# Kernel tuning notes

Hardware: AMD Instinct MI355X
Metric: run time of the kernel (lower is better)

The kernel has to match this reference:

```python
import jax, jax.numpy as jnp
import numpy as np

N = 4096  # num_dev == num_task (required by elementwise msg computation)
D = 64    # embed_dim


def setup_inputs() -> dict:
    key = jax.random.key(0)
    ks = jax.random.split(key, 10)
    return {
        "embed": jax.random.normal(ks[0], (2 * N, D), jnp.float32),
        "adj_collab": jnp.zeros((N, N), jnp.float32),   # only .shape[0] is used
        "adj_interact": jnp.zeros((N, N), jnp.float32),  # unused in forward body
        "adj_similar": jnp.zeros((N, N), jnp.float32),   # unused in forward body
        "collab_score": jax.random.normal(ks[1], (N, N), jnp.float32),
        "interact_score": jax.random.normal(ks[2], (N, N), jnp.float32),
        "similar_score": jax.random.normal(ks[3], (N, N), jnp.float32),
        "deg_dev": jax.random.uniform(ks[4], (N,), jnp.float32, 1.0, 100.0),
        "deg_task": jax.random.uniform(ks[5], (N,), jnp.float32, 1.0, 100.0),
        "W1": jax.random.normal(ks[6], (D, D), jnp.float32) / np.sqrt(D).astype(np.float32),
        "b1": jnp.zeros((D,), jnp.float32),
        "W2": jax.random.normal(ks[7], (D, D), jnp.float32) / np.sqrt(D).astype(np.float32),
        "b2": jnp.zeros((D,), jnp.float32),
        "W3": jax.random.normal(ks[8], (D, D), jnp.float32) / np.sqrt(D).astype(np.float32),
        "b3": jnp.zeros((D,), jnp.float32),
    }


def _linear(x, W, b):
    # torch nn.Linear: x @ W.T + b
    return x @ W.T + b


def _calc_attention(src, dst, rel_score, src_deg, dst_deg):
    # msg = dst + src*dst ; per-row dot <src, msg> ; degree + sqrt(d) scaling ; softmax
    msg = dst + src * dst                      # [N, D]
    dot = jnp.sum(src * msg, axis=-1)          # [N]
    scale = dot / (jnp.sqrt(src_deg * dst_deg + 1e-8) * jnp.sqrt(jnp.float32(src.shape[-1])))
    att = jax.nn.softmax(rel_score * scale, axis=-1)  # [N, N] (scale broadcasts over columns)
    return att, msg


def reference(embed, adj_collab, adj_interact, adj_similar,
              collab_score, interact_score, similar_score,
              deg_dev, deg_task, W1, b1, W2, b2, W3, b3):
    num_dev = adj_collab.shape[0]
    dev = embed[:num_dev]       # [N, D]
    task = embed[num_dev:]      # [N, D]

    collab_att, collab_msg = _calc_attention(dev, dev, collab_score, deg_dev, deg_dev)
    collab_prop = collab_att @ _linear(collab_msg, W1, b1)

    interact_att, interact_msg = _calc_attention(dev, task, interact_score, deg_dev, deg_task)
    interact_prop = interact_att @ _linear(interact_msg, W2, b2)

    dev_prop = jax.nn.leaky_relu(_linear(dev + collab_prop + interact_prop, W3, b3), 0.2)

    similar_att, _similar_msg = _calc_attention(task, task, similar_score, deg_task, deg_task)
    similar_prop = similar_att @ _linear(task, W3, b3)  # note: original uses W3(task_embed), not the msg
    task_prop = jax.nn.leaky_relu(_linear(task + similar_prop, W3, b3), 0.2)

    # dropout omitted (eval mode / identity)
    return jnp.concatenate([dev_prop, task_prop], axis=0)
```

## Files before the change

### kernel.cpp

```cpp
#include <hip/hip_runtime.h>
#include <math.h>

#define N 4096
#define D 64
#define NSLICE 4
#define JLEN 1024
#define CH 32
#define NCHUNK 32
#define SH 44.0f

#define S_OFF   0
#define MT_OFF  24576
#define E_OFF   36864
#define SCL_OFF 40960
#define LDS_BYTES 45056

typedef short bf16x8 __attribute__((ext_vector_type(8)));
typedef float f32x4  __attribute__((ext_vector_type(4)));

__device__ __forceinline__ unsigned short f2bf(float x) {
    unsigned int u = __float_as_uint(x);
    u += 0x7FFFu + ((u >> 16) & 1u);
    return (unsigned short)(u >> 16);
}
__device__ __forceinline__ float bf2f(unsigned short h) {
    return __uint_as_float(((unsigned int)h) << 16);
}

__device__ __forceinline__ void gld16(const void* g, void* l) {
    __builtin_amdgcn_global_load_lds(
        (const __attribute__((address_space(1))) void*)g,
        (__attribute__((address_space(3))) void*)l,
        16, 0, 0);
}

__device__ __forceinline__ void lds_barrier() {
    asm volatile("s_waitcnt lgkmcnt(0)" ::: "memory");
    __builtin_amdgcn_s_barrier();
    asm volatile("" ::: "memory");
}
__device__ __forceinline__ void plain_barrier() {
    asm volatile("" ::: "memory");
    __builtin_amdgcn_s_barrier();
    asm volatile("" ::: "memory");
}

__global__ __launch_bounds__(256) void prep_kernel(
    const float* __restrict__ embed,
    const float* __restrict__ degd, const float* __restrict__ degt,
    const float* __restrict__ W1, const float* __restrict__ b1,
    const float* __restrict__ W2, const float* __restrict__ b2,
    const float* __restrict__ W3, const float* __restrict__ b3,
    float* __restrict__ scale, unsigned short* __restrict__ Mt)
{
    const int rel = blockIdx.y;
    const float* W  = (rel == 0) ? W1 : (rel == 1 ? W2 : W3);
    const float* bb = (rel == 0) ? b1 : (rel == 1 ? b2 : b3);
    __shared__ float Wl[D][D + 1];
    __shared__ float xr[4][D];
    const int tid = threadIdx.x;
    for (int idx = tid; idx < D * D; idx += 256)
        Wl[idx >> 6][idx & 63] = W[idx];
    const int w = tid >> 6, d = tid & 63;
    const int i = blockIdx.x * 4 + w;

    float msg, term, xsrc, dga, dgb;
    if (rel == 0) {
        float s = embed[(size_t)i * D + d];
        msg = s + s * s; term = s * msg; xsrc = msg;
        dga = degd[i]; dgb = degd[i];
    } else if (rel == 1) {
        float s = embed[(size_t)i * D + d];
        float t = embed[(size_t)(N + i) * D + d];
        msg = t + s * t; term = s * msg; xsrc = msg;
        dga = degd[i]; dgb = degt[i];
    } else {
        float t = embed[(size_t)(N + i) * D + d];
        msg = t + t * t; term = t * msg; xsrc = t;
        dga = degt[i]; dgb = degt[i];
    }
    float dot = term;
    #pragma unroll
    for (int mm = 1; mm < 64; mm <<= 1) dot += __shfl_xor(dot, mm);
    if (d == 0)
        scale[rel * N + i] = dot / (sqrtf(dga * dgb + 1e-8f) * 8.0f);

    xr[w][d] = xsrc;
    __syncthreads();
    float o = bb[d];
    #pragma unroll 8
    for (int k = 0; k < D; ++k) o += xr[w][k] * Wl[d][k];
    Mt[((size_t)rel * D + d) * N + i] = f2bf(o);
}

__global__ __launch_bounds__(256, 3) void attn_kernel(
    const float* __restrict__ S0, const float* __restrict__ S1, const float* __restrict__ S2,
    const float* __restrict__ scale, const unsigned short* __restrict__ Mt,
    unsigned short* __restrict__ Up, float* __restrict__ lp)
{
    __shared__ __align__(16) char LDS[LDS_BYTES];
    const int rg = blockIdx.x, rel = blockIdx.y, sl = blockIdx.z;
    const float* S = (rel == 0) ? S0 : (rel == 1 ? S1 : S2);
    const unsigned short* Mtr = Mt + (size_t)rel * D * N;
    const int tid = threadIdx.x;
    const int lane = tid & 63, wave = tid >> 6;
    const int row = tid >> 2, q = tid & 3;
    const int j0 = sl * JLEN;

    const int srow = tid >> 3, sslot = tid & 7;
    const int sx = (sslot ^ (srow & 7)) * 4;
    const float* s0p = S + (size_t)(rg * 64 + srow) * N + j0 + sx;
    const float* s1p = S + (size_t)(rg * 64 + 32 + srow) * N + j0 + sx;
    const unsigned short* mtp = Mtr + (size_t)(tid & 63) * N + j0 + (tid >> 6) * 8;
    char* sldsw = LDS + S_OFF + wave * 1024;
    char* mldsw = LDS + MT_OFF + wave * 1024;

#define ISSUE(cc, bb) do {                                      \
        gld16(s0p + (cc) * CH, sldsw + (bb) * 8192);            \
        gld16(s1p + (cc) * CH, sldsw + (bb) * 8192 + 4096);     \
        gld16(mtp + (cc) * CH, mldsw + (bb) * 4096);            \
    } while (0)

    for (int k = tid; k < JLEN; k += 256)
        *(float*)(LDS + SCL_OFF + k * 4) = scale[rel * N + j0 + k];
    asm volatile("" ::: "memory");
    ISSUE(0, 0);
    ISSUE(1, 1);
    lds_barrier();

    const int wbase = wave * 16;
    const int lrow  = lane & 15;
    const int lk    = lane >> 4;
    float l = 0.f;
    f32x4 acc[4];
    #pragma unroll
    for (int ct = 0; ct < 4; ++ct) {
        acc[ct][0] = 0.f; acc[ct][1] = 0.f; acc[ct][2] = 0.f; acc[ct][3] = 0.f;
    }

    int bc = 0;
    for (int c = 0; c < NCHUNK; ++c) {
        if (c < NCHUNK - 1) asm volatile("s_waitcnt vmcnt(3)" ::: "memory");
        else                asm volatile("s_waitcnt vmcnt(0)" ::: "memory");
        plain_barrier();

        if (c + 2 < NCHUNK) {
            int bn = bc + 2; if (bn >= 3) bn -= 3;
            ISSUE(c + 2, bn);
        }

        {
            const char* sb = LDS + S_OFF + bc * 8192;
            const int r7 = row & 7;
            const f32x4 va = *(const f32x4*)(sb + row * 128 + (((2 * q)     ^ r7) << 4));
            const f32x4 vb = *(const f32x4*)(sb + row * 128 + (((2 * q + 1) ^ r7) << 4));
            const f32x4 ca = *(const f32x4*)(LDS + SCL_OFF + c * 128 + q * 32);
            const f32x4 cb = *(const f32x4*)(LDS + SCL_OFF + c * 128 + q * 32 + 16);
            float e[8];
            e[0] = __expf(fmaf(va[0], ca[0], -SH));
            e[1] = __expf(fmaf(va[1], ca[1], -SH));
            e[2] = __expf(fmaf(va[2], ca[2], -SH));
            e[3] = __expf(fmaf(va[3], ca[3], -SH));
            e[4] = __expf(fmaf(vb[0], cb[0], -SH));
            e[5] = __expf(fmaf(vb[1], cb[1], -SH));
            e[6] = __expf(fmaf(vb[2], cb[2], -SH));
            e[7] = __expf(fmaf(vb[3], cb[3], -SH));
            #pragma unroll
            for (int k = 0; k < 8; ++k) l += e[k];
            union { unsigned short h[8]; uint4 v; } pk;
            #pragma unroll
            for (int k = 0; k < 8; ++k) pk.h[k] = f2bf(e[k]);
            *(uint4*)(LDS + E_OFF + ((q * 64 + row) << 4)) = pk.v;
        }

        lds_barrier();

        {
            const char* mb = LDS + MT_OFF + bc * 4096;
            const bf16x8 a = *(const bf16x8*)(LDS + E_OFF + ((lk * 64 + wbase + lrow) << 4));
            #pragma unroll
            for (int ct = 0; ct < 4; ++ct) {
                const bf16x8 b = *(const bf16x8*)(mb + ((lk * 64 + ct * 16 + lrow) << 4));
                acc[ct] = __builtin_amdgcn_mfma_f32_16x16x32_bf16(a, b, acc[ct], 0, 0, 0);
            }
        }

        bc = bc + 1; if (bc == 3) bc = 0;
    }
#undef ISSUE

    unsigned short* R = (unsigned short*)LDS;
    #pragma unroll
    for (int ct = 0; ct < 4; ++ct)
        #pragma unroll
        for (int r = 0; r < 4; ++r) {
            const int ri = wbase + lk * 4 + r;
            R[ri * 64 + ct * 16 + lrow] = f2bf(acc[ct][r]);
        }
    lds_barrier();
    const size_t pbase = (size_t)((rel * 64 + rg) * NSLICE + sl);
    unsigned short* up = Up + pbase * 4096;
    {
        const uint4* src = (const uint4*)R;
        uint4*       dst = (uint4*)up;
        dst[tid]       = src[tid];
        dst[256 + tid] = src[256 + tid];
    }
    l += __shfl_xor(l, 1);
    l += __shfl_xor(l, 2);
    if (q == 0) lp[pbase * 64 + row] = l;
}

__device__ __forceinline__ float combine_row(
    const unsigned short* __restrict__ Up, const float* __restrict__ lp,
    int rel, int i, int d)
{
    const int rg = i >> 6, r = i & 63;
    const int base = (rel * 64 + rg) * NSLICE;
    float lt = 0.f, u = 0.f;
    #pragma unroll
    for (int p = 0; p < NSLICE; ++p) {
        lt += lp[(base + p) * 64 + r];
        u  += bf2f(Up[(size_t)(base + p) * 4096 + r * 64 + d]);
    }
    return u / lt;
}

__global__ __launch_bounds__(256) void final_kernel(
    const float* __restrict__ embed,
    const unsigned short* __restrict__ Up, const float* __restrict__ lp,
    const float* __restrict__ W3, const float* __restrict__ b3,
    float* __restrict__ out)
{
    __shared__ float Wl[D][D + 1];
    __shared__ float xs[4][D];
    const int tid = threadIdx.x;
    for (int idx = tid; idx < D * D; idx += 256)
        Wl[idx >> 6][idx & 63] = W3[idx];
    const int w = tid >> 6, d = tid & 63;
    const int g = blockIdx.x * 4 + w;

    float x = embed[(size_t)g * D + d];
    if (g < N) {
        x += combine_row(Up, lp, 0, g, d);
        x += combine_row(Up, lp, 1, g, d);
    } else {
        x += combine_row(Up, lp, 2, g - N, d);
    }
    xs[w][d] = x;
    __syncthreads();
    float o = b3[d];
    #pragma unroll 8
    for (int k = 0; k < D; ++k) o += xs[w][k] * Wl[d][k];
    o = (o > 0.f) ? o : 0.2f * o;
    out[(size_t)g * D + d] = o;
}

extern "C" void kernel_launch(void* const* d_in, const int* in_sizes, int n_in,
                              void* d_out, int out_size, void* d_ws, size_t ws_size,
                              hipStream_t stream)
{
    const float* embed = (const float*)d_in[0];
    const float* Sc   = (const float*)d_in[4];
    const float* Si   = (const float*)d_in[5];
    const float* Ss   = (const float*)d_in[6];
    const float* degd = (const float*)d_in[7];
    const float* degt = (const float*)d_in[8];
    const float* W1 = (const float*)d_in[9];
    const float* b1 = (const float*)d_in[10];
    const float* W2 = (const float*)d_in[11];
    const float* b2 = (const float*)d_in[12];
    const float* W3 = (const float*)d_in[13];
    const float* b3 = (const float*)d_in[14];
    float* out = (float*)d_out;

    float* ws    = (float*)d_ws;
    float* scale = ws;
    float* lp    = ws + 12288;
    unsigned short* Mt = (unsigned short*)(lp + 49152);
    unsigned short* Up = Mt + 786432;

    prep_kernel<<<dim3(N / 4, 3), 256, 0, stream>>>(
        embed, degd, degt, W1, b1, W2, b2, W3, b3, scale, Mt);
    attn_kernel<<<dim3(64, 3, NSLICE), 256, 0, stream>>>(
        Sc, Si, Ss, scale, Mt, Up, lp);
    final_kernel<<<dim3(2 * N / 4), 256, 0, stream>>>(
        embed, Up, lp, W3, b3, out);
}
```

Baseline: 59.97 us.

## Double column slices, deepen score prefetch to 4 buffers, swizzle E tile

Splits the column range into 8 slices instead of 4, so the attention grid has twice as many blocks, each covering half the columns. The score tiles get a 4-deep ring buffer with a 3-chunk lookahead, while the message tiles keep a 3-deep ring, and the wait counts are adjusted to match. The bf16 exponent tile in LDS is XOR-swizzled to reduce bank conflicts. The extra slices double the partial outputs that the final kernel must reduce, and the larger LDS footprint may lower occupancy.

Result: slower. 62.86 us (+4.8%).

```diff
diff --git a/kernel.cpp b/kernel.cpp
--- a/kernel.cpp
+++ b/kernel.cpp
@@ -3,17 +3,17 @@
 
 #define N 4096
 #define D 64
-#define NSLICE 4
-#define JLEN 1024
+#define NSLICE 8
+#define JLEN 512
 #define CH 32
-#define NCHUNK 32
+#define NCHUNK 16
 #define SH 44.0f
 
 #define S_OFF   0
-#define MT_OFF  24576
-#define E_OFF   36864
-#define SCL_OFF 40960
-#define LDS_BYTES 45056
+#define MT_OFF  32768
+#define E_OFF   45056
+#define SCL_OFF 49152
+#define LDS_BYTES 51200
 
 typedef short bf16x8 __attribute__((ext_vector_type(8)));
 typedef float f32x4  __attribute__((ext_vector_type(4)));
@@ -111,21 +111,22 @@
     const int sx = (sslot ^ (srow & 7)) * 4;
     const float* s0p = S + (size_t)(rg * 64 + srow) * N + j0 + sx;
     const float* s1p = S + (size_t)(rg * 64 + 32 + srow) * N + j0 + sx;
-    const unsigned short* mtp = Mtr + (size_t)(tid & 63) * N + j0 + (tid >> 6) * 8;
+    const unsigned short* mtp = Mtr + (size_t)(tid & 63) * N + j0 + wave * 8;
     char* sldsw = LDS + S_OFF + wave * 1024;
     char* mldsw = LDS + MT_OFF + wave * 1024;
 
-#define ISSUE(cc, bb) do {                                      \
-        gld16(s0p + (cc) * CH, sldsw + (bb) * 8192);            \
-        gld16(s1p + (cc) * CH, sldsw + (bb) * 8192 + 4096);     \
-        gld16(mtp + (cc) * CH, mldsw + (bb) * 4096);            \
+#define ISSUE_S(cc, bb) do {                                \
+        gld16(s0p + (cc) * CH, sldsw + (bb) * 8192);        \
+        gld16(s1p + (cc) * CH, sldsw + (bb) * 8192 + 4096); \
     } while (0)
+#define ISSUE_M(cc, bb) gld16(mtp + (cc) * CH, mldsw + (bb) * 4096)
 
     for (int k = tid; k < JLEN; k += 256)
         *(float*)(LDS + SCL_OFF + k * 4) = scale[rel * N + j0 + k];
     asm volatile("" ::: "memory");
-    ISSUE(0, 0);
-    ISSUE(1, 1);
+    ISSUE_M(0, 0); ISSUE_S(0, 0);
+    ISSUE_M(1, 1); ISSUE_S(1, 1);
+    ISSUE_S(2, 2);
     lds_barrier();
 
     const int wbase = wave * 16;
@@ -138,19 +139,18 @@
         acc[ct][0] = 0.f; acc[ct][1] = 0.f; acc[ct][2] = 0.f; acc[ct][3] = 0.f;
     }
 
-    int bc = 0;
+    int bm = 0;
     for (int c = 0; c < NCHUNK; ++c) {
-        if (c < NCHUNK - 1) asm volatile("s_waitcnt vmcnt(3)" ::: "memory");
-        else                asm volatile("s_waitcnt vmcnt(0)" ::: "memory");
+        if (c < NCHUNK - 2)       asm volatile("s_waitcnt vmcnt(5)" ::: "memory");
+        else if (c == NCHUNK - 2) asm volatile("s_waitcnt vmcnt(3)" ::: "memory");
+        else                      asm volatile("s_waitcnt vmcnt(0)" ::: "memory");
         plain_barrier();
 
-        if (c + 2 < NCHUNK) {
-            int bn = bc + 2; if (bn >= 3) bn -= 3;
-            ISSUE(c + 2, bn);
-        }
+        if (c + 2 < NCHUNK) { int t = bm + 2; if (t >= 3) t -= 3; ISSUE_M(c + 2, t); }
+        if (c + 3 < NCHUNK) ISSUE_S(c + 3, (c + 3) & 3);
 
         {
-            const char* sb = LDS + S_OFF + bc * 8192;
+            const char* sb = LDS + S_OFF + (c & 3) * 8192;
             const int r7 = row & 7;
             const f32x4 va = *(const f32x4*)(sb + row * 128 + (((2 * q)     ^ r7) << 4));
             const f32x4 vb = *(const f32x4*)(sb + row * 128 + (((2 * q + 1) ^ r7) << 4));
@@ -170,14 +170,15 @@
             union { unsigned short h[8]; uint4 v; } pk;
             #pragma unroll
             for (int k = 0; k < 8; ++k) pk.h[k] = f2bf(e[k]);
-            *(uint4*)(LDS + E_OFF + ((q * 64 + row) << 4)) = pk.v;
+            *(uint4*)(LDS + E_OFF + ((q * 64 + (row ^ (2 * q))) << 4)) = pk.v;
         }
 
         lds_barrier();
 
         {
-            const char* mb = LDS + MT_OFF + bc * 4096;
-            const bf16x8 a = *(const bf16x8*)(LDS + E_OFF + ((lk * 64 + wbase + lrow) << 4));
+            const char* mb = LDS + MT_OFF + bm * 4096;
+            const bf16x8 a = *(const bf16x8*)(
+                LDS + E_OFF + ((lk * 64 + ((wbase + lrow) ^ (2 * lk))) << 4));
             #pragma unroll
             for (int ct = 0; ct < 4; ++ct) {
                 const bf16x8 b = *(const bf16x8*)(mb + ((lk * 64 + ct * 16 + lrow) << 4));
@@ -185,9 +186,10 @@
             }
         }
 
-        bc = bc + 1; if (bc == 3) bc = 0;
-    }
-#undef ISSUE
+        bm = bm + 1; if (bm == 3) bm = 0;
+    }
+#undef ISSUE_S
+#undef ISSUE_M
 
     unsigned short* R = (unsigned short*)LDS;
     #pragma unroll
@@ -277,7 +279,7 @@
     float* ws    = (float*)d_ws;
     float* scale = ws;
     float* lp    = ws + 12288;
-    unsigned short* Mt = (unsigned short*)(lp + 49152);
+    unsigned short* Mt = (unsigned short*)(lp + 98304);
     unsigned short* Up = Mt + 786432;
 
     prep_kernel<<<dim3(N / 4, 3), 256, 0, stream>>>(
```
